# Performance work log

Measured on AMD Instinct MI355X. Metric: run time of the kernel, lower is better.

## Reference

```python
import jax, jax.numpy as jnp
import numpy as np

EPS = 1e-8


def householder_matrix(vs, dim):
    """Sequentially apply Householder reflections: Q <- (I - 2 v v^T / ||v||^2) Q."""
    def body(Q, v):
        coef = 2.0 / (jnp.sum(v * v) + EPS)
        Q = Q - coef * jnp.outer(v, v @ Q)
        return Q, None
    Q0 = jnp.eye(dim, dtype=vs.dtype)
    Q, _ = jax.lax.scan(body, Q0, vs)
    return Q


def _rotate_half(x):
    x1, x2 = jnp.split(x, 2, axis=-1)
    return jnp.concatenate((-x2, x1), axis=-1)


def setup_inputs() -> dict:
    key = jax.random.key(0)
    kq, kk, kc, ks, kv = jax.random.split(key, 5)
    B, H, S, D = 4, 16, 4096, 64
    q = jax.random.normal(kq, (B, H, S, D), dtype=jnp.float32)
    k = jax.random.normal(kk, (B, H, S, D), dtype=jnp.float32)
    cos = jax.random.uniform(kc, (B, S, D), dtype=jnp.float32)
    sin = jax.random.uniform(ks, (B, S, D), dtype=jnp.float32)
    vs = jax.random.normal(kv, (D // 2, D), dtype=jnp.float32) * 0.02
    return {"q": q, "k": k, "cos": cos, "sin": sin, "vs": vs}


def reference(q, k, cos, sin, vs):
    D = q.shape[-1]
    Q = householder_matrix(vs, D)            # [D, D], orthogonal
    # inverse rotation: x @ Q^T
    qi = q @ Q.T
    ki = k @ Q.T
    cos_b = cos[:, None, :, :]               # [B,1,S,D]
    sin_b = sin[:, None, :, :]
    q_rot = qi * cos_b + _rotate_half(qi) * sin_b
    k_rot = ki * cos_b + _rotate_half(ki) * sin_b
    # forward rotation: x @ Q
    return q_rot @ Q, k_rot @ Q
```

## Files before the change

kernel.cpp:

```cpp
#include <hip/hip_runtime.h>

typedef __attribute__((ext_vector_type(8))) short short8;
typedef __attribute__((ext_vector_type(4))) float floatx4;
typedef unsigned short u16;
typedef unsigned int   u32;

__device__ __forceinline__ u32 f2bf(float f) {
  u32 u = __float_as_uint(f);
  return (u + 0x7fffu + ((u >> 16) & 1u)) >> 16;
}

__device__ __forceinline__ short8 cvt8(const float* f) {
  short8 r;
#pragma unroll
  for (int j = 0; j < 8; j++) r[j] = (short)f2bf(f[j]);
  return r;
}

__global__ void __launch_bounds__(64) hh_kernel(const float* __restrict__ vs,
                                                u16* __restrict__ Qb,
                                                u16* __restrict__ Qtb) {
  const int j = threadIdx.x;
  float col[64];
#pragma unroll
  for (int i = 0; i < 64; i++) col[i] = (i == j) ? 1.f : 0.f;

  __shared__ float v[64];
#pragma unroll 1
  for (int r = 0; r < 32; r++) {
    __syncthreads();
    v[j] = vs[r * 64 + j];
    __syncthreads();
    float vv0 = 0, vv1 = 0, vv2 = 0, vv3 = 0, w0 = 0, w1 = 0, w2 = 0, w3 = 0;
#pragma unroll
    for (int i = 0; i < 64; i += 4) {
      float a0 = v[i], a1 = v[i + 1], a2 = v[i + 2], a3 = v[i + 3];
      vv0 += a0 * a0; vv1 += a1 * a1; vv2 += a2 * a2; vv3 += a3 * a3;
      w0 += a0 * col[i]; w1 += a1 * col[i + 1]; w2 += a2 * col[i + 2]; w3 += a3 * col[i + 3];
    }
    float coef = 2.f / (((vv0 + vv1) + (vv2 + vv3)) + 1e-8f);
    float cw = coef * ((w0 + w1) + (w2 + w3));
#pragma unroll
    for (int i = 0; i < 64; i++) col[i] -= v[i] * cw;
  }
#pragma unroll
  for (int i = 0; i < 64; i++) {
    Qb [i * 64 + j] = (u16)f2bf(col[i]);
    Qtb[j * 64 + i] = (u16)f2bf(col[i]);
  }
}

__global__ void __launch_bounds__(256) rnrope_kernel(
    const float* __restrict__ qp, const float* __restrict__ kp,
    const float* __restrict__ cosp, const float* __restrict__ sinp,
    const u16* __restrict__ Qb, const u16* __restrict__ Qtb,
    float* __restrict__ outp) {
  const int lane = threadIdx.x & 63;
  const int t    = lane & 15;
  const int quad = lane >> 4;
  const int wave = blockIdx.x * 4 + (threadIdx.x >> 6);

  __shared__ alignas(16) u16 sh_all[4][1152];
  u16* sh = sh_all[threadIdx.x >> 6];

  short8 aQ[4][2], aT[4][2];
#pragma unroll
  for (int i0 = 0; i0 < 4; i0++) {
#pragma unroll
    for (int ks = 0; ks < 2; ks++) {
      aQ[i0][ks] = *(const short8*)(Qb  + (i0 * 16 + t) * 64 + ks * 32 + quad * 8);
      aT[i0][ks] = *(const short8*)(Qtb + (i0 * 16 + t) * 64 + ks * 32 + quad * 8);
    }
  }

#pragma unroll 1
  for (int it = 0; it < 4; ++it) {
    const int tile = wave * 4 + it;
    const int tt   = tile & 16383;
    const bool isq = (tile < 16384);
    const float* __restrict__ inp = isq ? qp : kp;
    float* __restrict__ op = outp + (isq ? 0 : 16777216);
    const int token_base = tt * 16;
    const int s = token_base & 4095;
    const int b = token_base >> 16;
    const int csoff = ((b << 12) + s + t) * 64;
    const float* crow = cosp + csoff;
    const float* srow = sinp + csoff;
    const float* xrow = inp + (token_base + t) * 64;

    float xb[16];
    *(float4*)&xb[0]  = *(const float4*)(xrow + quad * 8);
    *(float4*)&xb[4]  = *(const float4*)(xrow + quad * 8 + 4);
    *(float4*)&xb[8]  = *(const float4*)(xrow + 32 + quad * 8);
    *(float4*)&xb[12] = *(const float4*)(xrow + 32 + quad * 8 + 4);
    short8 bq0 = cvt8(&xb[0]);
    short8 bq1 = cvt8(&xb[8]);

    floatx4 acc[4];
#pragma unroll
    for (int i0 = 0; i0 < 4; i0++) {
      floatx4 z = {0.f, 0.f, 0.f, 0.f};
      z = __builtin_amdgcn_mfma_f32_16x16x32_bf16(aQ[i0][0], bq0, z, 0, 0, 0);
      z = __builtin_amdgcn_mfma_f32_16x16x32_bf16(aQ[i0][1], bq1, z, 0, 0, 0);
      acc[i0] = z;
    }

    float4 c[4], sn[4];
#pragma unroll
    for (int i0 = 0; i0 < 4; i0++) {
      c [i0] = *(const float4*)(crow + i0 * 16 + quad * 4);
      sn[i0] = *(const float4*)(srow + i0 * 16 + quad * 4);
    }

#pragma unroll
    for (int i0 = 0; i0 < 4; i0++) {
      const int p = i0 ^ 2;
      const float sg = (i0 < 2) ? -1.f : 1.f;
      float r0 = acc[i0][0] * c[i0].x + sg * acc[p][0] * sn[i0].x;
      float r1 = acc[i0][1] * c[i0].y + sg * acc[p][1] * sn[i0].y;
      float r2 = acc[i0][2] * c[i0].z + sg * acc[p][2] * sn[i0].z;
      float r3 = acc[i0][3] * c[i0].w + sg * acc[p][3] * sn[i0].w;
      u32 lo = f2bf(r0) | (f2bf(r1) << 16);
      u32 hi = f2bf(r2) | (f2bf(r3) << 16);
      *(uint2*)&sh[t * 72 + i0 * 16 + quad * 4] = make_uint2(lo, hi);
    }

    __builtin_amdgcn_wave_barrier();
    short8 br0 = *(const short8*)&sh[t * 72 + quad * 8];
    short8 br1 = *(const short8*)&sh[t * 72 + 32 + quad * 8];

#pragma unroll
    for (int o0 = 0; o0 < 4; o0++) {
      floatx4 z = {0.f, 0.f, 0.f, 0.f};
      z = __builtin_amdgcn_mfma_f32_16x16x32_bf16(aT[o0][0], br0, z, 0, 0, 0);
      z = __builtin_amdgcn_mfma_f32_16x16x32_bf16(aT[o0][1], br1, z, 0, 0, 0);
      float4 st = make_float4(z[0], z[1], z[2], z[3]);
      *(float4*)(op + (token_base + t) * 64 + o0 * 16 + quad * 4) = st;
    }
    __builtin_amdgcn_wave_barrier();
  }
}

extern "C" void kernel_launch(void* const* d_in, const int* in_sizes, int n_in,
                              void* d_out, int out_size, void* d_ws, size_t ws_size,
                              hipStream_t stream) {
  const float* q    = (const float*)d_in[0];
  const float* k    = (const float*)d_in[1];
  const float* cosp = (const float*)d_in[2];
  const float* sinp = (const float*)d_in[3];
  const float* vs   = (const float*)d_in[4];
  float* out = (float*)d_out;
  u16* Qb  = (u16*)d_ws;
  u16* Qtb = Qb + 4096;

  hipLaunchKernelGGL(hh_kernel, dim3(1), dim3(64), 0, stream, vs, Qb, Qtb);
  hipLaunchKernelGGL(rnrope_kernel, dim3(2048), dim3(256), 0, stream,
                     q, k, cosp, sinp, Qb, Qtb, out);
}
```

Measured before the change: 307.2 us.

## Fuse Householder build into rope kernel and share cos/sin across heads

Removes the separate single-block Householder kernel by having each block rebuild Q and Q^T in shared memory from vs. Blocks are reorganized per (batch, 16-token tile) so cos/sin are loaded once into LDS and reused for all 16 heads of q and k. The next input tile is software-prefetched while the current one computes. The cost is redundant serial Householder computation in every block, plus MFMA operands read from LDS instead of registers.

```diff
diff --git a/kernel.cpp b/kernel.cpp
--- a/kernel.cpp
+++ b/kernel.cpp
@@ -10,132 +10,166 @@
   return (u + 0x7fffu + ((u >> 16) & 1u)) >> 16;
 }
 
-__device__ __forceinline__ short8 cvt8(const float* f) {
+__device__ __forceinline__ short8 cvt8v(float4 a, float4 b) {
   short8 r;
-#pragma unroll
-  for (int j = 0; j < 8; j++) r[j] = (short)f2bf(f[j]);
+  r[0] = (short)f2bf(a.x); r[1] = (short)f2bf(a.y); r[2] = (short)f2bf(a.z); r[3] = (short)f2bf(a.w);
+  r[4] = (short)f2bf(b.x); r[5] = (short)f2bf(b.y); r[6] = (short)f2bf(b.z); r[7] = (short)f2bf(b.w);
   return r;
 }
 
-__global__ void __launch_bounds__(64) hh_kernel(const float* __restrict__ vs,
-                                                u16* __restrict__ Qb,
-                                                u16* __restrict__ Qtb) {
-  const int j = threadIdx.x;
-  float col[64];
-#pragma unroll
-  for (int i = 0; i < 64; i++) col[i] = (i == j) ? 1.f : 0.f;
+#define QB_OFF  0
+#define QT_OFF  9216
+#define COS_OFF 18432
+#define SIN_OFF 22784
+#define SH_OFF  27136
+#define SV_OFF  18432
 
-  __shared__ float v[64];
-#pragma unroll 1
-  for (int r = 0; r < 32; r++) {
-    __syncthreads();
-    v[j] = vs[r * 64 + j];
-    __syncthreads();
-    float vv0 = 0, vv1 = 0, vv2 = 0, vv3 = 0, w0 = 0, w1 = 0, w2 = 0, w3 = 0;
-#pragma unroll
-    for (int i = 0; i < 64; i += 4) {
-      float a0 = v[i], a1 = v[i + 1], a2 = v[i + 2], a3 = v[i + 3];
-      vv0 += a0 * a0; vv1 += a1 * a1; vv2 += a2 * a2; vv3 += a3 * a3;
-      w0 += a0 * col[i]; w1 += a1 * col[i + 1]; w2 += a2 * col[i + 2]; w3 += a3 * col[i + 3];
-    }
-    float coef = 2.f / (((vv0 + vv1) + (vv2 + vv3)) + 1e-8f);
-    float cw = coef * ((w0 + w1) + (w2 + w3));
-#pragma unroll
-    for (int i = 0; i < 64; i++) col[i] -= v[i] * cw;
-  }
-#pragma unroll
-  for (int i = 0; i < 64; i++) {
-    Qb [i * 64 + j] = (u16)f2bf(col[i]);
-    Qtb[j * 64 + i] = (u16)f2bf(col[i]);
-  }
-}
-
-__global__ void __launch_bounds__(256) rnrope_kernel(
+__global__ void __launch_bounds__(256, 4) rnrope_fused(
     const float* __restrict__ qp, const float* __restrict__ kp,
     const float* __restrict__ cosp, const float* __restrict__ sinp,
-    const u16* __restrict__ Qb, const u16* __restrict__ Qtb,
-    float* __restrict__ outp) {
-  const int lane = threadIdx.x & 63;
+    const float* __restrict__ vsp, float* __restrict__ outp) {
+  __shared__ __align__(16) char smem[36352];
+  u16*   qb = (u16*)(smem + QB_OFF);
+  u16*   qt = (u16*)(smem + QT_OFF);
+  float* cs = (float*)(smem + COS_OFF);
+  float* sn = (float*)(smem + SIN_OFF);
+  float* sv = (float*)(smem + SV_OFF);
+
+  const int tid  = threadIdx.x;
+  const int lane = tid & 63;
   const int t    = lane & 15;
   const int quad = lane >> 4;
-  const int wave = blockIdx.x * 4 + (threadIdx.x >> 6);
+  const int wave = tid >> 6;
+  u16* shw = (u16*)(smem + SH_OFF) + wave * 1152;
 
-  __shared__ alignas(16) u16 sh_all[4][1152];
-  u16* sh = sh_all[threadIdx.x >> 6];
+  const int b  = blockIdx.x >> 8;
+  const int st = blockIdx.x & 255;
+  const int s  = st << 4;
 
-  short8 aQ[4][2], aT[4][2];
+  *(float4*)(sv + tid * 8)     = *(const float4*)(vsp + tid * 8);
+  *(float4*)(sv + tid * 8 + 4) = *(const float4*)(vsp + tid * 8 + 4);
+  const int tk  = tid >> 4;
+  const int off = (tid & 15) << 2;
+  const float4 creg = *(const float4*)(cosp + (((b << 12) + s + tk) << 6) + off);
+  const float4 sreg = *(const float4*)(sinp + (((b << 12) + s + tk) << 6) + off);
+  __syncthreads();
+
+  if (wave == 0) {
+    const int j = lane;
+    float col[64];
 #pragma unroll
-  for (int i0 = 0; i0 < 4; i0++) {
+    for (int i = 0; i < 64; i++) col[i] = (i == j) ? 1.f : 0.f;
+#pragma unroll 1
+    for (int r = 0; r < 32; r++) {
+      const float* vr = sv + r * 64;
+      float vv0 = 0, vv1 = 0, vv2 = 0, vv3 = 0, w0 = 0, w1 = 0, w2 = 0, w3 = 0;
 #pragma unroll
-    for (int ks = 0; ks < 2; ks++) {
-      aQ[i0][ks] = *(const short8*)(Qb  + (i0 * 16 + t) * 64 + ks * 32 + quad * 8);
-      aT[i0][ks] = *(const short8*)(Qtb + (i0 * 16 + t) * 64 + ks * 32 + quad * 8);
+      for (int i = 0; i < 64; i += 4) {
+        float4 v4 = *(const float4*)(vr + i);
+        vv0 += v4.x * v4.x; vv1 += v4.y * v4.y; vv2 += v4.z * v4.z; vv3 += v4.w * v4.w;
+        w0 += v4.x * col[i]; w1 += v4.y * col[i + 1]; w2 += v4.z * col[i + 2]; w3 += v4.w * col[i + 3];
+      }
+      float coef = 2.f / (((vv0 + vv1) + (vv2 + vv3)) + 1e-8f);
+      float cw = coef * ((w0 + w1) + (w2 + w3));
+#pragma unroll
+      for (int i = 0; i < 64; i += 4) {
+        float4 v4 = *(const float4*)(vr + i);
+        col[i]     -= v4.x * cw;
+        col[i + 1] -= v4.y * cw;
+        col[i + 2] -= v4.z * cw;
+        col[i + 3] -= v4.w * cw;
+      }
     }
+#pragma unroll
+    for (int i = 0; i < 64; i += 2) {
+      u16 v0 = (u16)f2bf(col[i]);
+      u16 v1 = (u16)f2bf(col[i + 1]);
+      qb[(i) * 72 + j]     = v0;
+      qb[(i + 1) * 72 + j] = v1;
+      *(u32*)&qt[j * 72 + i] = (u32)v0 | ((u32)v1 << 16);
+    }
+  }
+  __syncthreads();
+  *(float4*)(cs + tk * 68 + off) = creg;
+  *(float4*)(sn + tk * 68 + off) = sreg;
+  __syncthreads();
+
+  const int hbase = b << 4;
+  auto xptr = [&](int c) -> const float* {
+    const float* base = (c < 16) ? qp : kp;
+    return base + ((((hbase + (c & 15)) << 12) + s + t) << 6);
+  };
+
+  const int c0 = wave << 3;
+  float4 n0, n1, n2, n3;
+  {
+    const float* p = xptr(c0);
+    n0 = *(const float4*)(p + quad * 8);
+    n1 = *(const float4*)(p + quad * 8 + 4);
+    n2 = *(const float4*)(p + 32 + quad * 8);
+    n3 = *(const float4*)(p + 32 + quad * 8 + 4);
   }
 
 #pragma unroll 1
-  for (int it = 0; it < 4; ++it) {
-    const int tile = wave * 4 + it;
-    const int tt   = tile & 16383;
-    const bool isq = (tile < 16384);
-    const float* __restrict__ inp = isq ? qp : kp;
-    float* __restrict__ op = outp + (isq ? 0 : 16777216);
-    const int token_base = tt * 16;
-    const int s = token_base & 4095;
-    const int b = token_base >> 16;
-    const int csoff = ((b << 12) + s + t) * 64;
-    const float* crow = cosp + csoff;
-    const float* srow = sinp + csoff;
-    const float* xrow = inp + (token_base + t) * 64;
+  for (int it = 0; it < 8; ++it) {
+    const int c = c0 + it;
+    float4 x0 = n0, x1 = n1, x2 = n2, x3 = n3;
+    if (it < 7) {
+      const float* p = xptr(c + 1);
+      n0 = *(const float4*)(p + quad * 8);
+      n1 = *(const float4*)(p + quad * 8 + 4);
+      n2 = *(const float4*)(p + 32 + quad * 8);
+      n3 = *(const float4*)(p + 32 + quad * 8 + 4);
+    }
+    short8 bq0 = cvt8v(x0, x1);
+    short8 bq1 = cvt8v(x2, x3);
 
-    float xb[16];
-    *(float4*)&xb[0]  = *(const float4*)(xrow + quad * 8);
-    *(float4*)&xb[4]  = *(const float4*)(xrow + quad * 8 + 4);
-    *(float4*)&xb[8]  = *(const float4*)(xrow + 32 + quad * 8);
-    *(float4*)&xb[12] = *(const float4*)(xrow + 32 + quad * 8 + 4);
-    short8 bq0 = cvt8(&xb[0]);
-    short8 bq1 = cvt8(&xb[8]);
+    int qoff = 0;
+    asm volatile("" : "+v"(qoff));
 
     floatx4 acc[4];
 #pragma unroll
     for (int i0 = 0; i0 < 4; i0++) {
+      short8 a0 = *(const short8*)(qb + qoff + (i0 * 16 + t) * 72 + quad * 8);
+      short8 a1 = *(const short8*)(qb + qoff + (i0 * 16 + t) * 72 + 32 + quad * 8);
       floatx4 z = {0.f, 0.f, 0.f, 0.f};
-      z = __builtin_amdgcn_mfma_f32_16x16x32_bf16(aQ[i0][0], bq0, z, 0, 0, 0);
-      z = __builtin_amdgcn_mfma_f32_16x16x32_bf16(aQ[i0][1], bq1, z, 0, 0, 0);
+      z = __builtin_amdgcn_mfma_f32_16x16x32_bf16(a0, bq0, z, 0, 0, 0);
+      z = __builtin_amdgcn_mfma_f32_16x16x32_bf16(a1, bq1, z, 0, 0, 0);
       acc[i0] = z;
     }
 
-    float4 c[4], sn[4];
+    float4 c4[4], s4[4];
 #pragma unroll
     for (int i0 = 0; i0 < 4; i0++) {
-      c [i0] = *(const float4*)(crow + i0 * 16 + quad * 4);
-      sn[i0] = *(const float4*)(srow + i0 * 16 + quad * 4);
+      c4[i0] = *(const float4*)(cs + t * 68 + i0 * 16 + quad * 4);
+      s4[i0] = *(const float4*)(sn + t * 68 + i0 * 16 + quad * 4);
     }
-
 #pragma unroll
     for (int i0 = 0; i0 < 4; i0++) {
       const int p = i0 ^ 2;
       const float sg = (i0 < 2) ? -1.f : 1.f;
-      float r0 = acc[i0][0] * c[i0].x + sg * acc[p][0] * sn[i0].x;
-      float r1 = acc[i0][1] * c[i0].y + sg * acc[p][1] * sn[i0].y;
-      float r2 = acc[i0][2] * c[i0].z + sg * acc[p][2] * sn[i0].z;
-      float r3 = acc[i0][3] * c[i0].w + sg * acc[p][3] * sn[i0].w;
+      float r0 = acc[i0][0] * c4[i0].x + sg * acc[p][0] * s4[i0].x;
+      float r1 = acc[i0][1] * c4[i0].y + sg * acc[p][1] * s4[i0].y;
+      float r2 = acc[i0][2] * c4[i0].z + sg * acc[p][2] * s4[i0].z;
+      float r3 = acc[i0][3] * c4[i0].w + sg * acc[p][3] * s4[i0].w;
       u32 lo = f2bf(r0) | (f2bf(r1) << 16);
       u32 hi = f2bf(r2) | (f2bf(r3) << 16);
-      *(uint2*)&sh[t * 72 + i0 * 16 + quad * 4] = make_uint2(lo, hi);
+      *(uint2*)&shw[t * 72 + i0 * 16 + quad * 4] = make_uint2(lo, hi);
     }
 
     __builtin_amdgcn_wave_barrier();
-    short8 br0 = *(const short8*)&sh[t * 72 + quad * 8];
-    short8 br1 = *(const short8*)&sh[t * 72 + 32 + quad * 8];
+    short8 br0 = *(const short8*)&shw[t * 72 + quad * 8];
+    short8 br1 = *(const short8*)&shw[t * 72 + 32 + quad * 8];
 
+    float* op = outp + ((c < 16) ? 0 : 16777216) + ((((hbase + (c & 15)) << 12) + s + t) << 6);
 #pragma unroll
     for (int o0 = 0; o0 < 4; o0++) {
+      short8 a0 = *(const short8*)(qt + qoff + (o0 * 16 + t) * 72 + quad * 8);
+      short8 a1 = *(const short8*)(qt + qoff + (o0 * 16 + t) * 72 + 32 + quad * 8);
       floatx4 z = {0.f, 0.f, 0.f, 0.f};
-      z = __builtin_amdgcn_mfma_f32_16x16x32_bf16(aT[o0][0], br0, z, 0, 0, 0);
-      z = __builtin_amdgcn_mfma_f32_16x16x32_bf16(aT[o0][1], br1, z, 0, 0, 0);
-      float4 st = make_float4(z[0], z[1], z[2], z[3]);
-      *(float4*)(op + (token_base + t) * 64 + o0 * 16 + quad * 4) = st;
+      z = __builtin_amdgcn_mfma_f32_16x16x32_bf16(a0, br0, z, 0, 0, 0);
+      z = __builtin_amdgcn_mfma_f32_16x16x32_bf16(a1, br1, z, 0, 0, 0);
+      *(float4*)(op + o0 * 16 + quad * 4) = make_float4(z[0], z[1], z[2], z[3]);
     }
     __builtin_amdgcn_wave_barrier();
   }
@@ -150,10 +184,6 @@
   const float* sinp = (const float*)d_in[3];
   const float* vs   = (const float*)d_in[4];
   float* out = (float*)d_out;
-  u16* Qb  = (u16*)d_ws;
-  u16* Qtb = Qb + 4096;
-
-  hipLaunchKernelGGL(hh_kernel, dim3(1), dim3(64), 0, stream, vs, Qb, Qtb);
-  hipLaunchKernelGGL(rnrope_kernel, dim3(2048), dim3(256), 0, stream,
-                     q, k, cosp, sinp, Qb, Qtb, out);
+  hipLaunchKernelGGL(rnrope_fused, dim3(1024), dim3(256), 0, stream,
+                     q, k, cosp, sinp, vs, out);
 }
```

Measured after the change: 304.9 us. Within noise of the previous version (-0.8%).
